# Kernel optimization log

Hardware: AMD Instinct MI355X
Metric: run time of the kernel (lower is better)

The kernel has to match this reference:

```python
import jax, jax.numpy as jnp
import numpy as np
import math

B, S, H, NH = 8, 2048, 128, 4
DH = H // NH
SQRT_2_OVER_PI = math.sqrt(2.0 / math.pi)


def layer_norm(x, a, b, eps=1e-6):
    # Faithful to the torch module: unbiased std (ddof=1) and divide by (std + eps)
    mean = jnp.mean(x, axis=-1, keepdims=True)
    std = jnp.std(x, axis=-1, keepdims=True, ddof=1)
    return a * (x - mean) / (std + eps) + b


def setup_inputs() -> dict:
    key = jax.random.key(0)
    ks = jax.random.split(key, 10)
    inp = {
        "hidden": jax.random.normal(ks[0], (B, S, H), dtype=jnp.float32),
        "mask": jax.random.randint(ks[1], (B, S), 0, 2, dtype=jnp.int32),
        # attention params
        "attn_scale_w": jax.random.normal(ks[2], (NH, S), dtype=jnp.float32) * 0.1,
        "Wl": jax.random.normal(ks[3], (H, H), dtype=jnp.float32) * (1.0 / math.sqrt(H)),
        "bl": jnp.zeros((H,), dtype=jnp.float32),
        # FFN params
        "W1": jax.random.normal(ks[4], (H, H), dtype=jnp.float32) * (1.0 / math.sqrt(H)),
        "b1": jnp.zeros((H,), dtype=jnp.float32),
        "ffn_scale_w": jax.random.normal(ks[5], (S, 1), dtype=jnp.float32) * 0.1,
        # layer norms
        "ln1_a": jnp.ones((H,), dtype=jnp.float32),
        "ln1_b": jnp.zeros((H,), dtype=jnp.float32),
        "ln2_a": jnp.ones((H,), dtype=jnp.float32),
        "ln2_b": jnp.zeros((H,), dtype=jnp.float32),
    }
    return inp


def reference(hidden, mask, attn_scale_w, Wl, bl, W1, b1, ffn_scale_w,
              ln1_a, ln1_b, ln2_a, ln2_b):
    x = hidden  # [B, S, H]

    # --- attention sublayer (pre-norm residual) ---
    n1 = layer_norm(x, ln1_a, ln1_b)
    qkv = n1.reshape(B, S, NH, DH).transpose(0, 2, 1, 3)  # [B, NH, S, DH]
    # scores with per-head/per-query-position learned scale
    corr = jnp.einsum("bhqd,bhkd->bhqk", qkv, qkv) / math.sqrt(DH)
    corr = corr * attn_scale_w[None, :, :, None]  # scale over query positions
    # mask over key positions: [B,1,1,S], broadcast matches repeat in torch
    corr = jnp.where(mask[:, None, None, :] == 0, -1e9, corr)
    prob = jax.nn.softmax(corr, axis=-1)
    h = jnp.einsum("bhqk,bhkd->bhqd", prob, qkv)
    h = h.transpose(0, 2, 1, 3).reshape(B, S, H)
    attn_out = h @ Wl.T + bl
    x = x + attn_out

    # --- FFN sublayer (pre-norm residual) ---
    n2 = layer_norm(x, ln2_a, ln2_b)
    hf = ffn_scale_w[None] * (n2 @ W1.T + b1)  # [B, S, H] with per-position scale
    act = 0.5 * hf * (1.0 + jnp.tanh(SQRT_2_OVER_PI * (hf + 0.044715 * hf ** 3)))
    x = x + act

    return x
```

## Files before the change

kernel.cpp:

```cpp
#include <hip/hip_runtime.h>

#define BB 8
#define SS 2048
#define HH 128
#define NHH 4
#define DHH 32

typedef _Float16 f16;
typedef f16 f16x4 __attribute__((ext_vector_type(4)));
typedef f16 f16x8 __attribute__((ext_vector_type(8)));
typedef float f32x4 __attribute__((ext_vector_type(4)));

__device__ __forceinline__ f16x8 cat(f16x4 a, f16x4 b) {
  return (f16x8){a[0], a[1], a[2], a[3], b[0], b[1], b[2], b[3]};
}

__device__ __forceinline__ f16x4 tr_read(const f16* p) {
  f16x4 d;
  asm volatile("ds_read_b64_tr_b16 %0, %1"
               : "=v"(d)
               : "v"((__attribute__((address_space(3))) const f16*)p)
               : "memory");
  return d;
}

__global__ __launch_bounds__(256) void stage1_kernel(const float* __restrict__ x,
                                                     const float* __restrict__ ga,
                                                     const float* __restrict__ gb,
                                                     const float* __restrict__ Wl,
                                                     const float* __restrict__ W1,
                                                     const int* __restrict__ mask,
                                                     f16* __restrict__ n1,
                                                     f16* __restrict__ Wlf,
                                                     f16* __restrict__ W1f,
                                                     int* __restrict__ idx,
                                                     int* __restrict__ nkcnt,
                                                     int* __restrict__ nkpad) {
  const int tid = threadIdx.x;
  if (blockIdx.x < 1024) {
    const int wave = tid >> 6, lane = tid & 63;
    const int grp = lane >> 4, lm = lane & 15;
    const int r = wave * 4 + grp;
    const size_t row = (size_t)blockIdx.x * 16 + r;

    const float* xr = x + row * HH + lm * 8;
    float4 v0 = *(const float4*)(xr);
    float4 v1 = *(const float4*)(xr + 4);
    float xv[8] = {v0.x, v0.y, v0.z, v0.w, v1.x, v1.y, v1.z, v1.w};
    float sum = 0.f, sq = 0.f;
#pragma unroll
    for (int j = 0; j < 8; ++j) { sum += xv[j]; sq += xv[j] * xv[j]; }
#pragma unroll
    for (int m = 1; m < 16; m <<= 1) {
      sum += __shfl_xor(sum, m);
      sq += __shfl_xor(sq, m);
    }
    float mean = sum * (1.0f / HH);
    float var = fmaxf((sq - (float)HH * mean * mean) * (1.0f / (HH - 1)), 0.0f);
    float inv = 1.0f / (sqrtf(var) + 1e-6f);

    float4 a0 = *(const float4*)(ga + lm * 8);
    float4 a1 = *(const float4*)(ga + lm * 8 + 4);
    float4 b0 = *(const float4*)(gb + lm * 8);
    float4 b1 = *(const float4*)(gb + lm * 8 + 4);
    float av[8] = {a0.x, a0.y, a0.z, a0.w, a1.x, a1.y, a1.z, a1.w};
    float bv[8] = {b0.x, b0.y, b0.z, b0.w, b1.x, b1.y, b1.z, b1.w};
    f16x8 w;
#pragma unroll
    for (int j = 0; j < 8; ++j) w[j] = (f16)(av[j] * (xv[j] - mean) * inv + bv[j]);
    *(f16x8*)(n1 + row * HH + lm * 8) = w;
    return;
  }
  if (blockIdx.x < 1056) {
    int g = (blockIdx.x - 1024) * 256 + tid;
    if (g < 4096) {
      float4 w = ((const float4*)Wl)[g];
      f16x4 o = {(f16)w.x, (f16)w.y, (f16)w.z, (f16)w.w};
      ((f16x4*)Wlf)[g] = o;
    } else {
      float4 w = ((const float4*)W1)[g - 4096];
      f16x4 o = {(f16)w.x, (f16)w.y, (f16)w.z, (f16)w.w};
      ((f16x4*)W1f)[g - 4096] = o;
    }
    return;
  }
  const int b = blockIdx.x - 1056;
  __shared__ int ps[256];
  int m8[8];
  int cnt = 0;
  const int* mp = mask + b * SS + tid * 8;
#pragma unroll
  for (int j = 0; j < 8; ++j) {
    m8[j] = mp[j];
    cnt += (m8[j] != 0);
  }
  ps[tid] = cnt;
  __syncthreads();
  for (int off = 1; off < 256; off <<= 1) {
    int v = (tid >= off) ? ps[tid - off] : 0;
    __syncthreads();
    ps[tid] += v;
    __syncthreads();
  }
  int pos = ps[tid] - cnt;
#pragma unroll
  for (int j = 0; j < 8; ++j) {
    if (m8[j] != 0) idx[b * SS + pos++] = tid * 8 + j;
  }
  __syncthreads();
  int nkv = ps[255];
  int npv = (nkv + 63) & ~63;
  if (npv == 0) npv = 64;
  for (int jj = nkv + tid; jj < npv; jj += 256) idx[b * SS + jj] = 0;
  if (tid == 255) { nkcnt[b] = nkv; nkpad[b] = npv; }
}

__global__ __launch_bounds__(256, 2) void attn_kernel(const f16* __restrict__ n1,
                                                      const int* __restrict__ idx,
                                                      const int* __restrict__ nkcnt,
                                                      const int* __restrict__ nkpad,
                                                      const float* __restrict__ scalew,
                                                      f16* __restrict__ hatt) {
  const int tid = threadIdx.x;
  const int b = blockIdx.x & 7;
  const int qb = (blockIdx.x >> 3) & 15;
  const int h = blockIdx.x >> 7;
  const int wave = tid >> 6, lane = tid & 63;
  const int lg = lane >> 4, lm = lane & 15;
  const int nk = nkcnt[b];
  const int ns = nkpad[b] >> 6;

  __shared__ __align__(16) f16 Kt[4][2][2][64][16];
  __shared__ __align__(16) int idxL[SS];

  const f16* __restrict__ nb = n1 + (size_t)b * SS * HH + h * DHH;
  f16* __restrict__ tile = &Kt[wave][0][0][0][0];

  for (int j = tid * 4; j < (ns << 6); j += 1024)
    *(int4*)&idxL[j] = *(const int4*)(idx + b * SS + j);

  const int q0 = qb * 128 + wave * 32 + lm;
  f16x8 qf[2];
#pragma unroll
  for (int qt = 0; qt < 2; ++qt) {
    int q = q0 + qt * 16;
    f16x8 raw = *(const f16x8*)(nb + (size_t)q * HH + lg * 8);
    f16 s = (f16)(scalew[h * SS + q] * 0.2550680718664f);
#pragma unroll
    for (int j = 0; j < 8; ++j) raw[j] *= s;
    qf[qt] = raw;
  }

  const int sk = lane >> 2, sp = lane & 3;

  const f32x4 zero = {0.f, 0.f, 0.f, 0.f};
  f32x4 acc[2][2] = {{zero, zero}, {zero, zero}};
  f32x4 lacc[2] = {zero, zero};
  const f16x8 ones = {(f16)1, (f16)1, (f16)1, (f16)1, (f16)1, (f16)1, (f16)1, (f16)1};

  __syncthreads();

#pragma unroll
  for (int i = 0; i < 4; ++i) {
    int row = idxL[i * 16 + sk];
    f16x8 v = *(const f16x8*)(nb + (size_t)row * HH + sp * 8);
    *(f16x8*)(tile + (sp >> 1) * 1024 + (i * 16 + sk) * 16 + (sp & 1) * 8) = v;
  }

  for (int c = 0; c < ns; ++c) {
    const int bo = (c & 1) * 2048;
    const int k0 = c * 64;
    f16x8 kreg[4];
    const bool more = (c + 1 < ns);
    if (more) {
#pragma unroll
      for (int i = 0; i < 4; ++i) {
        int row = idxL[k0 + 64 + i * 16 + sk];
        kreg[i] = *(const f16x8*)(nb + (size_t)row * HH + sp * 8);
      }
    }

    f16x4 t0a = tr_read(tile + bo + 0 + lane * 4);
    f16x4 t0b = tr_read(tile + bo + 256 + lane * 4);
    f16x4 t0c = tr_read(tile + bo + 512 + lane * 4);
    f16x4 t0d = tr_read(tile + bo + 768 + lane * 4);
    f16x4 t1a = tr_read(tile + bo + 1024 + lane * 4);
    f16x4 t1b = tr_read(tile + bo + 1280 + lane * 4);
    f16x4 t1c = tr_read(tile + bo + 1536 + lane * 4);
    f16x4 t1d = tr_read(tile + bo + 1792 + lane * 4);

    f16x8 kf[4];
#pragma unroll
    for (int t = 0; t < 4; ++t)
      kf[t] = *(const f16x8*)(tile + bo + (lg >> 1) * 1024 + (t * 16 + lm) * 16 + (lg & 1) * 8);

    const bool tail = (k0 + 64 > nk);
    f16x8 pf[2][2];
#define PF_LOOP(MASKED)                                                                   \
  _Pragma("unroll") for (int qt = 0; qt < 2; ++qt) {                                      \
    _Pragma("unroll") for (int t = 0; t < 4; ++t) {                                       \
      f32x4 st = __builtin_amdgcn_mfma_f32_16x16x32_f16(kf[t], qf[qt], zero, 0, 0, 0);    \
      _Pragma("unroll") for (int r = 0; r < 4; ++r) {                                     \
        float pe = __builtin_amdgcn_exp2f(st[r]);                                         \
        if (MASKED && (k0 + t * 16 + lg * 4 + r >= nk)) pe = 0.0f;                        \
        pf[qt][t >> 1][(t & 1) * 4 + r] = (f16)pe;                                        \
      }                                                                                   \
    }                                                                                     \
  }
    if (!tail) { PF_LOOP(false) } else { PF_LOOP(true) }
#undef PF_LOOP

#pragma unroll
    for (int qt = 0; qt < 2; ++qt) {
#pragma unroll
      for (int s = 0; s < 2; ++s)
        lacc[qt] = __builtin_amdgcn_mfma_f32_16x16x32_f16(ones, pf[qt][s], lacc[qt], 0, 0, 0);
    }

    asm volatile("s_waitcnt lgkmcnt(0)" ::: "memory");
    __builtin_amdgcn_sched_barrier(0);

    f16x8 vf;
    vf = cat(t0a, t0b);
#pragma unroll
    for (int qt = 0; qt < 2; ++qt)
      acc[qt][0] = __builtin_amdgcn_mfma_f32_16x16x32_f16(vf, pf[qt][0], acc[qt][0], 0, 0, 0);
    vf = cat(t1a, t1b);
#pragma unroll
    for (int qt = 0; qt < 2; ++qt)
      acc[qt][1] = __builtin_amdgcn_mfma_f32_16x16x32_f16(vf, pf[qt][0], acc[qt][1], 0, 0, 0);
    vf = cat(t0c, t0d);
#pragma unroll
    for (int qt = 0; qt < 2; ++qt)
      acc[qt][0] = __builtin_amdgcn_mfma_f32_16x16x32_f16(vf, pf[qt][1], acc[qt][0], 0, 0, 0);
    vf = cat(t1c, t1d);
#pragma unroll
    for (int qt = 0; qt < 2; ++qt)
      acc[qt][1] = __builtin_amdgcn_mfma_f32_16x16x32_f16(vf, pf[qt][1], acc[qt][1], 0, 0, 0);

    if (more) {
      const int bn = 2048 - (c & 1) * 2048;
#pragma unroll
      for (int i = 0; i < 4; ++i)
        *(f16x8*)(tile + bn + (sp >> 1) * 1024 + (i * 16 + sk) * 16 + (sp & 1) * 8) = kreg[i];
    }
  }

#pragma unroll
  for (int qt = 0; qt < 2; ++qt) {
    float inv = 1.0f / lacc[qt][0];
    int q = q0 + qt * 16;
    f16* op = hatt + (size_t)(b * SS + q) * HH + h * DHH;
    f16x4 o0 = {(f16)(acc[qt][0][0] * inv), (f16)(acc[qt][0][1] * inv),
                (f16)(acc[qt][0][2] * inv), (f16)(acc[qt][0][3] * inv)};
    f16x4 o1 = {(f16)(acc[qt][1][0] * inv), (f16)(acc[qt][1][1] * inv),
                (f16)(acc[qt][1][2] * inv), (f16)(acc[qt][1][3] * inv)};
    *(f16x4*)(op + lg * 4) = o0;
    *(f16x4*)(op + 16 + lg * 4) = o1;
  }
}

__global__ __launch_bounds__(256) void mlp_kernel(const f16* __restrict__ X,
                                                  const f16* __restrict__ Wlf,
                                                  const float* __restrict__ bl,
                                                  const float* __restrict__ resid,
                                                  const float* __restrict__ ln2a,
                                                  const float* __restrict__ ln2b,
                                                  const f16* __restrict__ W1f,
                                                  const float* __restrict__ b1,
                                                  const float* __restrict__ fscale,
                                                  float* __restrict__ out) {
  const int tid = threadIdx.x;
  const int wave = tid >> 6, lane = tid & 63;
  const int lg = lane >> 4, lm = lane & 15;
  const int rbase = blockIdx.x * 32;
  const int nc0 = wave * 32;

  __shared__ __align__(16) f16 n2t[32][136];
  __shared__ float red[4][32][2];

  f32x4 acc[2][2] = {};
  const f16* xr0 = X + (size_t)(rbase + lm) * HH;
  const f16* xr1 = X + (size_t)(rbase + 16 + lm) * HH;
#pragma unroll
  for (int ks = 0; ks < 4; ++ks) {
    f16x8 bf0 = *(const f16x8*)(xr0 + ks * 32 + lg * 8);
    f16x8 bf1 = *(const f16x8*)(xr1 + ks * 32 + lg * 8);
#pragma unroll
    for (int nt = 0; nt < 2; ++nt) {
      f16x8 af = *(const f16x8*)(Wlf + (size_t)(nc0 + nt * 16 + lm) * HH + ks * 32 + lg * 8);
      acc[0][nt] = __builtin_amdgcn_mfma_f32_16x16x32_f16(af, bf0, acc[0][nt], 0, 0, 0);
      acc[1][nt] = __builtin_amdgcn_mfma_f32_16x16x32_f16(af, bf1, acc[1][nt], 0, 0, 0);
    }
  }
  float sum[2] = {0.f, 0.f}, sq[2] = {0.f, 0.f};
  f32x4 o[2][2];
#pragma unroll
  for (int g = 0; g < 2; ++g) {
    int row = rbase + g * 16 + lm;
#pragma unroll
    for (int nt = 0; nt < 2; ++nt) {
      int n = nc0 + nt * 16 + lg * 4;
      float4 rv = *(const float4*)(resid + (size_t)row * HH + n);
      float4 bv = *(const float4*)(bl + n);
      f32x4 v = acc[g][nt];
      v[0] += rv.x + bv.x; v[1] += rv.y + bv.y;
      v[2] += rv.z + bv.z; v[3] += rv.w + bv.w;
      o[g][nt] = v;
      sum[g] += v[0] + v[1] + v[2] + v[3];
      sq[g] += v[0] * v[0] + v[1] * v[1] + v[2] * v[2] + v[3] * v[3];
    }
    sum[g] += __shfl_xor(sum[g], 16); sum[g] += __shfl_xor(sum[g], 32);
    sq[g] += __shfl_xor(sq[g], 16);  sq[g] += __shfl_xor(sq[g], 32);
  }
  if (lane < 16) {
#pragma unroll
    for (int g = 0; g < 2; ++g) {
      red[wave][g * 16 + lm][0] = sum[g];
      red[wave][g * 16 + lm][1] = sq[g];
    }
  }
  __syncthreads();
#pragma unroll
  for (int g = 0; g < 2; ++g) {
    int lr = g * 16 + lm;
    float ts = red[0][lr][0] + red[1][lr][0] + red[2][lr][0] + red[3][lr][0];
    float tq = red[0][lr][1] + red[1][lr][1] + red[2][lr][1] + red[3][lr][1];
    float mean = ts * (1.0f / HH);
    float var = fmaxf((tq - (float)HH * mean * mean) * (1.0f / (HH - 1)), 0.0f);
    float inv = 1.0f / (sqrtf(var) + 1e-6f);
#pragma unroll
    for (int nt = 0; nt < 2; ++nt) {
      int n = nc0 + nt * 16 + lg * 4;
      float4 av = *(const float4*)(ln2a + n);
      float4 b2 = *(const float4*)(ln2b + n);
      f16x4 w;
      w[0] = (f16)(av.x * (o[g][nt][0] - mean) * inv + b2.x);
      w[1] = (f16)(av.y * (o[g][nt][1] - mean) * inv + b2.y);
      w[2] = (f16)(av.z * (o[g][nt][2] - mean) * inv + b2.z);
      w[3] = (f16)(av.w * (o[g][nt][3] - mean) * inv + b2.w);
      *(f16x4*)(&n2t[lr][n]) = w;
    }
  }
  __syncthreads();

  f32x4 fa[2][2] = {};
#pragma unroll
  for (int ks = 0; ks < 4; ++ks) {
    f16x8 bf0 = *(const f16x8*)(&n2t[lm][ks * 32 + lg * 8]);
    f16x8 bf1 = *(const f16x8*)(&n2t[16 + lm][ks * 32 + lg * 8]);
#pragma unroll
    for (int nt = 0; nt < 2; ++nt) {
      f16x8 af = *(const f16x8*)(W1f + (size_t)(nc0 + nt * 16 + lm) * HH + ks * 32 + lg * 8);
      fa[0][nt] = __builtin_amdgcn_mfma_f32_16x16x32_f16(af, bf0, fa[0][nt], 0, 0, 0);
      fa[1][nt] = __builtin_amdgcn_mfma_f32_16x16x32_f16(af, bf1, fa[1][nt], 0, 0, 0);
    }
  }
#pragma unroll
  for (int g = 0; g < 2; ++g) {
    int row = rbase + g * 16 + lm;
    float fs = fscale[row & (SS - 1)];
#pragma unroll
    for (int nt = 0; nt < 2; ++nt) {
      int n = nc0 + nt * 16 + lg * 4;
      float4 bv = *(const float4*)(b1 + n);
      const float* bp = &bv.x;
#pragma unroll
      for (int e = 0; e < 4; ++e) {
        float hf = fs * (fa[g][nt][e] + bp[e]);
        float u = 0.7978845608028654f * hf * (1.0f + 0.044715f * hf * hf);
        float ex = __builtin_amdgcn_exp2f(u * 2.8853900817779268f);
        float t = 1.0f - 2.0f / (ex + 1.0f);
        o[g][nt][e] += 0.5f * hf * (1.0f + t);
      }
      *(f32x4*)(out + (size_t)row * HH + n) = o[g][nt];
    }
  }
}

extern "C" void kernel_launch(void* const* d_in, const int* in_sizes, int n_in,
                              void* d_out, int out_size, void* d_ws, size_t ws_size,
                              hipStream_t stream) {
  const float* hidden = (const float*)d_in[0];
  const int* mask = (const int*)d_in[1];
  const float* scalew = (const float*)d_in[2];
  const float* Wl = (const float*)d_in[3];
  const float* bl = (const float*)d_in[4];
  const float* W1 = (const float*)d_in[5];
  const float* b1 = (const float*)d_in[6];
  const float* fscale = (const float*)d_in[7];
  const float* ln1a = (const float*)d_in[8];
  const float* ln1b = (const float*)d_in[9];
  const float* ln2a = (const float*)d_in[10];
  const float* ln2b = (const float*)d_in[11];
  float* out = (float*)d_out;

  const size_t NE = (size_t)BB * SS * HH;
  f16* n1 = (f16*)d_ws;
  f16* hattf = n1 + NE;
  f16* Wlf = hattf + NE;
  f16* W1f = Wlf + HH * HH;
  int* idx = (int*)(W1f + HH * HH);
  int* nkcnt = idx + BB * SS;
  int* nkpad = nkcnt + BB;

  stage1_kernel<<<1064, 256, 0, stream>>>(hidden, ln1a, ln1b, Wl, W1, mask,
                                          n1, Wlf, W1f, idx, nkcnt, nkpad);
  attn_kernel<<<BB * NHH * (SS / 128), 256, 0, stream>>>(n1, idx, nkcnt, nkpad,
                                                         scalew, hattf);
  mlp_kernel<<<BB * SS / 32, 256, 0, stream>>>(hattf, Wlf, bl, hidden, ln2a, ln2b,
                                               W1f, b1, fscale, out);
}
```

Baseline: 39.41 us.

## Split attention key range across two blocks and merge with a combine kernel

The attention kernel now splits each block's key chunks into two halves, doubling the grid so each block handles half the keys. Each half writes a normalized partial output plus its softmax denominator to a workspace. A new combine kernel then merges the two halves using denominator weights. Launch bounds are also raised to allow more resident blocks per CU. The aim is better CU fill and latency hiding, at the cost of an extra launch and extra global traffic for the partial results.

Result: slower. 42.94 us (+9.0%).

```diff
diff --git a/kernel.cpp b/kernel.cpp
--- a/kernel.cpp
+++ b/kernel.cpp
@@ -115,26 +115,31 @@
   if (tid == 255) { nkcnt[b] = nkv; nkpad[b] = npv; }
 }
 
-__global__ __launch_bounds__(256, 2) void attn_kernel(const f16* __restrict__ n1,
+__global__ __launch_bounds__(256, 4) void attn_kernel(const f16* __restrict__ n1,
                                                       const int* __restrict__ idx,
                                                       const int* __restrict__ nkcnt,
                                                       const int* __restrict__ nkpad,
                                                       const float* __restrict__ scalew,
-                                                      f16* __restrict__ hatt) {
+                                                      f16* __restrict__ pnum,
+                                                      float* __restrict__ pden) {
   const int tid = threadIdx.x;
   const int b = blockIdx.x & 7;
   const int qb = (blockIdx.x >> 3) & 15;
-  const int h = blockIdx.x >> 7;
+  const int h = (blockIdx.x >> 7) & 3;
+  const int ks = blockIdx.x >> 9;
   const int wave = tid >> 6, lane = tid & 63;
   const int lg = lane >> 4, lm = lane & 15;
   const int nk = nkcnt[b];
   const int ns = nkpad[b] >> 6;
-
-  __shared__ __align__(16) f16 Kt[4][2][2][64][16];
+  const int hc = (ns + 1) >> 1;
+  const int c0 = ks * hc;
+  const int c1 = (c0 + hc < ns) ? c0 + hc : ns;
+
+  __shared__ __align__(16) f16 Kt[4][2][2048];
   __shared__ __align__(16) int idxL[SS];
 
   const f16* __restrict__ nb = n1 + (size_t)b * SS * HH + h * DHH;
-  f16* __restrict__ tile = &Kt[wave][0][0][0][0];
+  f16* __restrict__ tile = &Kt[wave][0][0];
 
   for (int j = tid * 4; j < (ns << 6); j += 1024)
     *(int4*)&idxL[j] = *(const int4*)(idx + b * SS + j);
@@ -160,18 +165,20 @@
 
   __syncthreads();
 
-#pragma unroll
-  for (int i = 0; i < 4; ++i) {
-    int row = idxL[i * 16 + sk];
-    f16x8 v = *(const f16x8*)(nb + (size_t)row * HH + sp * 8);
-    *(f16x8*)(tile + (sp >> 1) * 1024 + (i * 16 + sk) * 16 + (sp & 1) * 8) = v;
-  }
-
-  for (int c = 0; c < ns; ++c) {
+  if (c0 < c1) {
+#pragma unroll
+    for (int i = 0; i < 4; ++i) {
+      int row = idxL[c0 * 64 + i * 16 + sk];
+      f16x8 v = *(const f16x8*)(nb + (size_t)row * HH + sp * 8);
+      *(f16x8*)(tile + (c0 & 1) * 2048 + (sp >> 1) * 1024 + (i * 16 + sk) * 16 + (sp & 1) * 8) = v;
+    }
+  }
+
+  for (int c = c0; c < c1; ++c) {
     const int bo = (c & 1) * 2048;
     const int k0 = c * 64;
     f16x8 kreg[4];
-    const bool more = (c + 1 < ns);
+    const bool more = (c + 1 < c1);
     if (more) {
 #pragma unroll
       for (int i = 0; i < 4; ++i) {
@@ -248,16 +255,39 @@
 
 #pragma unroll
   for (int qt = 0; qt < 2; ++qt) {
-    float inv = 1.0f / lacc[qt][0];
+    float den = lacc[qt][0];
+    float inv = (den > 0.f) ? 1.0f / den : 0.f;
     int q = q0 + qt * 16;
-    f16* op = hatt + (size_t)(b * SS + q) * HH + h * DHH;
+    size_t row = (size_t)ks * BB * SS + (size_t)b * SS + q;
+    f16* op = pnum + row * HH + h * DHH;
     f16x4 o0 = {(f16)(acc[qt][0][0] * inv), (f16)(acc[qt][0][1] * inv),
                 (f16)(acc[qt][0][2] * inv), (f16)(acc[qt][0][3] * inv)};
     f16x4 o1 = {(f16)(acc[qt][1][0] * inv), (f16)(acc[qt][1][1] * inv),
                 (f16)(acc[qt][1][2] * inv), (f16)(acc[qt][1][3] * inv)};
     *(f16x4*)(op + lg * 4) = o0;
     *(f16x4*)(op + 16 + lg * 4) = o1;
-  }
+    if (lg == 0) pden[row] = den;
+  }
+}
+
+__global__ __launch_bounds__(256) void combine_kernel(const f16* __restrict__ pnum,
+                                                      const float* __restrict__ pden,
+                                                      f16* __restrict__ hatt) {
+  const int blk = blockIdx.x;
+  const int b = blk & 7;
+  const int r0 = (blk >> 3) * 16;
+  const int tid = threadIdx.x;
+  const size_t row = (size_t)b * SS + r0 + (tid >> 4);
+  const int cg = (tid & 15) * 8;
+  float d0 = pden[row], d1 = pden[(size_t)BB * SS + row];
+  float inv = 1.0f / (d0 + d1);
+  float w0 = d0 * inv, w1 = d1 * inv;
+  f16x8 a = *(const f16x8*)(pnum + row * HH + cg);
+  f16x8 c = *(const f16x8*)(pnum + ((size_t)BB * SS + row) * HH + cg);
+  f16x8 o;
+#pragma unroll
+  for (int j = 0; j < 8; ++j) o[j] = (f16)(w0 * (float)a[j] + w1 * (float)c[j]);
+  *(f16x8*)(hatt + row * HH + cg) = o;
 }
 
 __global__ __launch_bounds__(256) void mlp_kernel(const f16* __restrict__ X,
@@ -398,16 +428,19 @@
   const size_t NE = (size_t)BB * SS * HH;
   f16* n1 = (f16*)d_ws;
   f16* hattf = n1 + NE;
-  f16* Wlf = hattf + NE;
+  f16* pnum = hattf + NE;
+  f16* Wlf = pnum + 2 * NE;
   f16* W1f = Wlf + HH * HH;
-  int* idx = (int*)(W1f + HH * HH);
+  float* pden = (float*)(W1f + HH * HH);
+  int* idx = (int*)(pden + 2 * BB * SS);
   int* nkcnt = idx + BB * SS;
   int* nkpad = nkcnt + BB;
 
   stage1_kernel<<<1064, 256, 0, stream>>>(hidden, ln1a, ln1b, Wl, W1, mask,
                                           n1, Wlf, W1f, idx, nkcnt, nkpad);
-  attn_kernel<<<BB * NHH * (SS / 128), 256, 0, stream>>>(n1, idx, nkcnt, nkpad,
-                                                         scalew, hattf);
+  attn_kernel<<<2 * BB * NHH * (SS / 128), 256, 0, stream>>>(n1, idx, nkcnt, nkpad,
+                                                             scalew, pnum, pden);
+  combine_kernel<<<1024, 256, 0, stream>>>(pnum, pden, hattf);
   mlp_kernel<<<BB * SS / 32, 256, 0, stream>>>(hattf, Wlf, bl, hidden, ln2a, ln2b,
                                                W1f, b1, fscale, out);
 }
```
